# Kernel tuning notes

Measured on AMD Instinct MI355X. Metric: run time of the kernel, lower is better.

## Reference

```python
import jax, jax.numpy as jnp
import numpy as np

N = 8388608  # batch size
RANGE = 0.02  # self.range in the original module


def setup_inputs() -> dict:
    key = jax.random.key(0)
    k1, k2 = jax.random.split(key)
    preds = jax.random.uniform(k1, (N, 3), dtype=jnp.float32)
    # target is binary ground truth (conditions compare against 0 and 1)
    target = jax.random.randint(k2, (N, 3), 0, 2).astype(jnp.float32)
    return {"preds": preds, "target": target}


def reference(preds, target):
    # Vectorized translation of the per-row scalar branching in RangeLoss.forward.
    p0, p1, p2 = preds[:, 0], preds[:, 1], preds[:, 2]
    t0, t1, t2 = target[:, 0], target[:, 1], target[:, 2]

    # columns 0 and 2: snap target to pred when pred is confidently correct
    t0 = jnp.where((p0 < 0.1) & (t0 == 0.0), p0, t0)
    t0 = jnp.where((p0 > 0.9) & (t0 == 1.0), p0, t0)
    t2 = jnp.where((p2 < 0.1) & (t2 == 0.0), p2, t2)
    t2 = jnp.where((p2 > 0.9) & (t2 == 1.0), p2, t2)

    # column 1: if preds[:,2] > 0.9 take pred; elif pred within +/-RANGE of target take pred
    in_range = (p1 * (1.0 + RANGE) > t1) & (p1 * (1.0 - RANGE) < t1)
    t1 = jnp.where(p2 > 0.9, p1, jnp.where(in_range, p1, t1))

    tgt = jnp.stack([t0, t1, t2], axis=1)  # [N, 3]
    # use_log=False, reduce='mean' in the module defaults
    return jnp.mean((preds - tgt) ** 2)
```

## Files before the change

kernel.cpp:

```cpp
#include <hip/hip_runtime.h>


#define N3      25165824
#define G4      6291456
#define BLOCK   256
#define UNROLL  4
#define INV_TOTAL (1.0f / 25165824.0f)

__global__ void __launch_bounds__(BLOCK) rangeloss_kernel(
    const float4* __restrict__ preds4,
    const float4* __restrict__ target4,
    const float*  __restrict__ predsf,
    float* __restrict__ out)
{
    const int base = blockIdx.x * (BLOCK * UNROLL) + threadIdx.x;

    float4 p[UNROLL], t[UNROLL];
    float  pn[UNROLL];

    #pragma unroll
    for (int k = 0; k < UNROLL; ++k) {
        const int i = base + k * BLOCK;
        p[k] = preds4[i];
        t[k] = target4[i];
        const int nf = 4 * i + 4;
        pn[k] = predsf[nf < N3 ? nf : 0];
    }

    float sum = 0.0f;

    #pragma unroll
    for (int k = 0; k < UNROLL; ++k) {
        const int i  = base + k * BLOCK;
        const int c0 = (4 * i) % 3;

        const float pe[4]  = {p[k].x, p[k].y, p[k].z, p[k].w};
        const float te[4]  = {t[k].x, t[k].y, t[k].z, t[k].w};
        const float pnx[4] = {p[k].y, p[k].z, p[k].w, pn[k]};

        #pragma unroll
        for (int e = 0; e < 4; ++e) {
            int col = c0 + e;
            col = (col >= 3) ? col - 3 : col;

            const float pp = pe[e], tt = te[e];

            const bool rule02 = (pp < 0.1f && tt == 0.0f) || (pp > 0.9f && tt == 1.0f);
            const bool rule1  = (pnx[e] > 0.9f) || (pp * 1.02f > tt && pp * 0.98f < tt);
            const bool snap   = (col == 1) ? rule1 : rule02;

            const float tn = snap ? pp : tt;
            const float d  = pp - tn;
            sum += d * d;
        }
    }

    sum *= INV_TOTAL;

    #pragma unroll
    for (int off = 32; off > 0; off >>= 1)
        sum += __shfl_down(sum, off, 64);

    __shared__ float smem[BLOCK / 64];
    const int lane = threadIdx.x & 63;
    const int wave = threadIdx.x >> 6;
    if (lane == 0) smem[wave] = sum;
    __syncthreads();

    if (threadIdx.x == 0) {
        atomicAdd(out, smem[0] + smem[1] + smem[2] + smem[3]);
    }
}

extern "C" void kernel_launch(void* const* d_in, const int* in_sizes, int n_in,
                              void* d_out, int out_size, void* d_ws, size_t ws_size,
                              hipStream_t stream)
{
    const float4* preds4  = (const float4*)d_in[0];
    const float4* target4 = (const float4*)d_in[1];
    const float*  predsf  = (const float*)d_in[0];
    float* out = (float*)d_out;

    hipMemsetAsync(out, 0, sizeof(float), stream);

    const int n_blocks = G4 / (BLOCK * UNROLL);
    rangeloss_kernel<<<n_blocks, BLOCK, 0, stream>>>(preds4, target4, predsf, out);
}
```

Before: 232.2 us.

## Replace atomic reduction with two-stage partials and shuffle neighbor loads

The single atomicAdd-per-block reduction and memset are replaced by a stage-1 kernel that writes one partial sum per block into the workspace, followed by a single-block stage-2 kernel that sums the partials. The extra scalar load of the next element per float4 is replaced by a wavefront shuffle, with only lane 63 doing a global load. This removes 6144 same-address atomics, the memset and redundant gather loads. The cost is a second kernel launch.

Result: faster. 216.7 us (-6.7%).

```diff
diff --git a/kernel.cpp b/kernel.cpp
--- a/kernel.cpp
+++ b/kernel.cpp
@@ -5,38 +5,44 @@
 #define G4      6291456
 #define BLOCK   256
 #define UNROLL  4
+#define NBLOCKS (G4 / (BLOCK * UNROLL))
 #define INV_TOTAL (1.0f / 25165824.0f)
 
-__global__ void __launch_bounds__(BLOCK) rangeloss_kernel(
+__global__ void __launch_bounds__(BLOCK) rangeloss_stage1(
     const float4* __restrict__ preds4,
     const float4* __restrict__ target4,
     const float*  __restrict__ predsf,
-    float* __restrict__ out)
+    float* __restrict__ partials)
 {
     const int base = blockIdx.x * (BLOCK * UNROLL) + threadIdx.x;
+    const int lane = threadIdx.x & 63;
 
     float4 p[UNROLL], t[UNROLL];
-    float  pn[UNROLL];
 
     #pragma unroll
     for (int k = 0; k < UNROLL; ++k) {
         const int i = base + k * BLOCK;
         p[k] = preds4[i];
         t[k] = target4[i];
-        const int nf = 4 * i + 4;
-        pn[k] = predsf[nf < N3 ? nf : 0];
     }
 
     float sum = 0.0f;
 
     #pragma unroll
     for (int k = 0; k < UNROLL; ++k) {
-        const int i  = base + k * BLOCK;
-        const int c0 = (4 * i) % 3;
+        const int i = base + k * BLOCK;
+
+        float pnext = __shfl_down(p[k].x, 1, 64);
+        if (lane == 63) {
+            const int nf = 4 * i + 4;
+            pnext = predsf[nf < N3 ? nf : 0];
+        }
 
         const float pe[4]  = {p[k].x, p[k].y, p[k].z, p[k].w};
         const float te[4]  = {t[k].x, t[k].y, t[k].z, t[k].w};
-        const float pnx[4] = {p[k].y, p[k].z, p[k].w, pn[k]};
+        const float pnx[4] = {p[k].y, p[k].z, p[k].w, pnext};
+
+        const int c0 = (4 * i) % 3;
 
         #pragma unroll
         for (int e = 0; e < 4; ++e) {
@@ -62,14 +68,34 @@
         sum += __shfl_down(sum, off, 64);
 
     __shared__ float smem[BLOCK / 64];
+    const int wave = threadIdx.x >> 6;
+    if (lane == 0) smem[wave] = sum;
+    __syncthreads();
+
+    if (threadIdx.x == 0)
+        partials[blockIdx.x] = smem[0] + smem[1] + smem[2] + smem[3];
+}
+
+__global__ void __launch_bounds__(BLOCK) rangeloss_stage2(
+    const float* __restrict__ partials,
+    float* __restrict__ out)
+{
+    float sum = 0.0f;
+    for (int i = threadIdx.x; i < NBLOCKS; i += BLOCK)
+        sum += partials[i];
+
+    #pragma unroll
+    for (int off = 32; off > 0; off >>= 1)
+        sum += __shfl_down(sum, off, 64);
+
+    __shared__ float smem[BLOCK / 64];
     const int lane = threadIdx.x & 63;
     const int wave = threadIdx.x >> 6;
     if (lane == 0) smem[wave] = sum;
     __syncthreads();
 
-    if (threadIdx.x == 0) {
-        atomicAdd(out, smem[0] + smem[1] + smem[2] + smem[3]);
-    }
+    if (threadIdx.x == 0)
+        out[0] = smem[0] + smem[1] + smem[2] + smem[3];
 }
 
 extern "C" void kernel_launch(void* const* d_in, const int* in_sizes, int n_in,
@@ -79,10 +105,9 @@
     const float4* preds4  = (const float4*)d_in[0];
     const float4* target4 = (const float4*)d_in[1];
     const float*  predsf  = (const float*)d_in[0];
+    float* partials = (float*)d_ws;
     float* out = (float*)d_out;
 
-    hipMemsetAsync(out, 0, sizeof(float), stream);
-
-    const int n_blocks = G4 / (BLOCK * UNROLL);
-    rangeloss_kernel<<<n_blocks, BLOCK, 0, stream>>>(preds4, target4, predsf, out);
+    rangeloss_stage1<<<NBLOCKS, BLOCK, 0, stream>>>(preds4, target4, predsf, partials);
+    rangeloss_stage2<<<1, BLOCK, 0, stream>>>(partials, out);
 }
```
